# Performance work log

Measured on AMD Instinct MI355X. Metric: run time of the kernel, lower is better.

## Reference

```python
import jax, jax.numpy as jnp
import numpy as np

D_MODEL = 1024
STATE_DIM = 128


def setup_inputs() -> dict:
    key = jax.random.key(0)
    ks = jax.random.split(key, 8)
    B, T, D, N = 8, 4096, D_MODEL, STATE_DIM
    u = jax.random.normal(ks[0], (B, T, D), dtype=jnp.float32)
    h0 = jnp.zeros((B, N), dtype=jnp.float32)
    log_A = jax.random.normal(ks[1], (N,), dtype=jnp.float32) * 0.1 - 1.0
    B_w = jax.random.normal(ks[2], (N, D), dtype=jnp.float32) / np.sqrt(D)
    B_b = jax.random.normal(ks[3], (N,), dtype=jnp.float32) * 0.01
    C_w = jax.random.normal(ks[4], (D, N), dtype=jnp.float32) / np.sqrt(N)
    C_b = jax.random.normal(ks[5], (D,), dtype=jnp.float32) * 0.01
    D_param = jnp.ones((D,), dtype=jnp.float32) * 0.1
    log_dt = jax.random.normal(ks[6], (N,), dtype=jnp.float32) * 0.1 - 2.0
    return {"u": u, "h0": h0, "log_A": log_A, "B_w": B_w, "B_b": B_b,
            "C_w": C_w, "C_b": C_b, "D_param": D_param, "log_dt": log_dt}


def reference(u, h0, log_A, B_w, B_b, C_w, C_b, D_param, log_dt):
    # u: [B, T, D], h0: [B, N]
    dt = jnp.minimum(jnp.exp(log_dt), 1.0)          # [N]
    A = -jnp.exp(log_A)                             # [N]
    A_bar = jnp.exp(A * dt)                         # [N]
    # B_bar * u, precomputed for all timesteps: [B, T, N]
    Bu = (jnp.einsum('btd,nd->btn', u, B_w) + B_b) * dt

    def step(h, bu_t):
        h = A_bar * h + bu_t                        # [B, N]
        return h, h

    # scan over time: Bu transposed to [T, B, N]
    _, hs = jax.lax.scan(step, h0, jnp.swapaxes(Bu, 0, 1))
    hs = jnp.swapaxes(hs, 0, 1)                     # [B, T, N]
    # y = C h + c_bias + D * u
    y = jnp.einsum('btn,dn->btd', hs, C_w) + C_b + D_param * u
    return y
```

## Files before the change

### kernel.cpp

```cpp
#include <hip/hip_runtime.h>

#define B_SZ 8
#define T_SZ 4096
#define D_SZ 1024
#define N_SZ 128
#define M_SZ (B_SZ*T_SZ)
#define CHUNK 64
#define NCHUNK (T_SZ/CHUNK)

typedef __attribute__((ext_vector_type(8))) __bf16 bf16x8;
typedef __attribute__((ext_vector_type(4))) float f32x4;
typedef __attribute__((ext_vector_type(4))) unsigned int u32x4;
typedef __attribute__((ext_vector_type(4))) float fvec4;

static __device__ __forceinline__ unsigned short f2bf(float f){
  union { float f; unsigned int u; } v; v.f = f;
  unsigned int r = v.u + 0x7fffu + ((v.u >> 16) & 1u);
  return (unsigned short)(r >> 16);
}

static __device__ __forceinline__ float bf2f(unsigned short s){
  union { unsigned int u; float f; } v; v.u = ((unsigned)s) << 16;
  return v.f;
}

static __device__ __forceinline__ void cp16(const void* g, void* l){
  __builtin_amdgcn_global_load_lds(
      (const __attribute__((address_space(1))) void*)g,
      (__attribute__((address_space(3))) void*)l, 16, 0, 0);
}

static __device__ __forceinline__ f32x4 zero4(){
  f32x4 v = {0.f, 0.f, 0.f, 0.f};
  return v;
}

__global__ __launch_bounds__(256) void k_conv(const float* __restrict__ Bw,
                                              const float* __restrict__ Cw,
                                              unsigned short* __restrict__ bw,
                                              unsigned short* __restrict__ cw){
  int t = blockIdx.x*256 + threadIdx.x;
  {
    int n = t >> 10, k = t & 1023;
    int c = k >> 6, kk = k & 63;
    unsigned byte = (unsigned)c*16384u + (unsigned)n*128u
                  + (unsigned)((kk*2) ^ ((n&7)<<4));
    bw[byte>>1] = f2bf(Bw[n*1024 + k]);
  }
  {
    int d = t >> 7, k = t & 127;
    int c = d >> 7, dd = d & 127;
    unsigned byte = (unsigned)c*32768u + (unsigned)dd*256u
                  + (unsigned)((k*2) ^ ((dd&15)<<4));
    cw[byte>>1] = f2bf(Cw[d*128 + k]);
  }
}

__global__ __launch_bounds__(256) void k_gemm1c(const float* __restrict__ u,
                                                const unsigned short* __restrict__ bw,
                                                const float* __restrict__ Bb,
                                                const float* __restrict__ logA,
                                                const float* __restrict__ logdt,
                                                unsigned short* __restrict__ Bu_bf,
                                                float* __restrict__ carry){
  __shared__ __align__(16) char smem[32768];
  unsigned short* lA = (unsigned short*)smem;
  unsigned short* lB = (unsigned short*)(smem + 8192);
  float*          BuT = (float*)smem;
  const int tid  = threadIdx.x;
  const int lane = tid & 63;
  const int wave = tid >> 6;
  const int bc   = blockIdx.x;
  const int m0   = bc * 64;
  const int l15  = lane & 15;
  const int lhi  = lane >> 4;

  f32x4 acc[8];
  #pragma unroll
  for (int i=0;i<8;++i) acc[i] = zero4();

  for (int kc=0; kc<16; ++kc){
    #pragma unroll
    for (int rep=0; rep<4; ++rep){
      const char* g = (const char*)bw + kc*16384 + rep*4096 + wave*1024 + lane*16;
      char* l = (char*)lB + rep*4096 + wave*1024;
      cp16(g, l);
    }
    #pragma unroll
    for (int rep=0; rep<2; ++rep){
      int q = rep*256 + tid;
      int row = q >> 3, ks = q & 7;
      const float* src = u + (size_t)(m0+row)*1024 + kc*64 + ks*8;
      fvec4 f0 = *(const fvec4*)src;
      fvec4 f1 = *(const fvec4*)(src+4);
      u32x4 p;
      p.x = (unsigned)f2bf(f0.x) | ((unsigned)f2bf(f0.y)<<16);
      p.y = (unsigned)f2bf(f0.z) | ((unsigned)f2bf(f0.w)<<16);
      p.z = (unsigned)f2bf(f1.x) | ((unsigned)f2bf(f1.y)<<16);
      p.w = (unsigned)f2bf(f1.z) | ((unsigned)f2bf(f1.w)<<16);
      unsigned byte = (unsigned)row*128u + (unsigned)((ks*16) ^ ((row&7)<<4));
      *(u32x4*)((char*)lA + byte) = p;
    }
    __syncthreads();
    #pragma unroll
    for (int k0=0; k0<64; k0+=32){
      int arow = wave*16 + l15;
      int ak = k0 + lhi*8;
      bf16x8 af = *(const bf16x8*)((const char*)lA + arow*128 + ((ak*2) ^ ((arow&7)<<4)));
      #pragma unroll
      for (int ct=0; ct<8; ++ct){
        int bn = ct*16 + l15;
        bf16x8 bfv = *(const bf16x8*)((const char*)lB + bn*128 + ((ak*2) ^ ((bn&7)<<4)));
        acc[ct] = __builtin_amdgcn_mfma_f32_16x16x32_bf16(af, bfv, acc[ct], 0, 0, 0);
      }
    }
    __syncthreads();
  }

  #pragma unroll
  for (int ct=0; ct<8; ++ct){
    int n = ct*16 + l15;
    float dt = fminf(__expf(logdt[n]), 1.f);
    float bb = Bb[n];
    #pragma unroll
    for (int r=0;r<4;++r){
      int ml = wave*16 + lhi*4 + r;
      BuT[ml*128 + n] = (acc[ct][r] + bb) * dt;
    }
  }
  __syncthreads();

  #pragma unroll
  for (int i=0;i<4;++i){
    int q = i*256 + tid;
    const float* s = BuT + q*8;
    fvec4 a = *(const fvec4*)s;
    fvec4 b = *(const fvec4*)(s+4);
    u32x4 p;
    p.x = (unsigned)f2bf(a.x) | ((unsigned)f2bf(a.y)<<16);
    p.y = (unsigned)f2bf(a.z) | ((unsigned)f2bf(a.w)<<16);
    p.z = (unsigned)f2bf(b.x) | ((unsigned)f2bf(b.y)<<16);
    p.w = (unsigned)f2bf(b.z) | ((unsigned)f2bf(b.w)<<16);
    *(u32x4*)((char*)Bu_bf + (size_t)bc*16384 + (size_t)q*16) = p;
  }

  if (tid < 128){
    int n = tid;
    float dt = fminf(__expf(logdt[n]), 1.f);
    float Ab = __expf(-__expf(logA[n]) * dt);
    float h = 0.f;
    #pragma unroll 8
    for (int j=0;j<CHUNK;++j) h = fmaf(Ab, h, BuT[j*128 + n]);
    carry[(size_t)bc*128 + n] = h;
  }
}

__global__ __launch_bounds__(256) void k_gemm2s(const unsigned short* __restrict__ Bu_bf,
                                                const float* __restrict__ carry,
                                                const unsigned short* __restrict__ cw,
                                                const float* __restrict__ u,
                                                const float* __restrict__ h0,
                                                const float* __restrict__ Cb,
                                                const float* __restrict__ Dp,
                                                const float* __restrict__ logA,
                                                const float* __restrict__ logdt,
                                                float* __restrict__ y){
  __shared__ __align__(16) unsigned short BuT[64*128];
  __shared__ __align__(16) unsigned short hsT[64*128];
  __shared__ __align__(16) unsigned short cwT[128*128];
  const int tid = threadIdx.x, lane = tid & 63, wave = tid >> 6;
  const int bc = blockIdx.x;
  const int m0 = bc * 64;
  const int l15 = lane & 15, lhi = lane >> 4;

  #pragma unroll
  for (int i=0;i<4;++i){
    int off = i*4096 + tid*16;
    cp16((const char*)Bu_bf + (size_t)bc*16384 + off, (char*)BuT + off);
  }
  #pragma unroll
  for (int i=0;i<8;++i){
    int off = i*4096 + tid*16;
    cp16((const char*)cw + off, (char*)cwT + off);
  }

  float hreg = 0.f, Ab = 0.f;
  if (tid < 128){
    int n = tid;
    int b = bc >> 6, c = bc & 63;
    float dt = fminf(__expf(logdt[n]), 1.f);
    float Ad = -__expf(logA[n]) * dt;
    Ab = __expf(Ad);
    float AL = __expf(Ad * (float)CHUNK);
    float h = h0[b*128 + n];
    for (int i=0;i<c;++i)
      h = fmaf(AL, h, carry[(size_t)(b*NCHUNK + i)*128 + n]);
    hreg = h;
  }
  __syncthreads();

  if (tid < 128){
    int n = tid;
    float h = hreg;
    #pragma unroll 8
    for (int j=0;j<CHUNK;++j){
      h = fmaf(Ab, h, bf2f(BuT[j*128 + n]));
      unsigned byte = (unsigned)j*256u + (unsigned)((n*2) ^ ((j&15)<<4));
      *(unsigned short*)((char*)hsT + byte) = f2bf(h);
    }
  }
  __syncthreads();

  for (int d=0; d<8; ++d){
    f32x4 acc[8];
    #pragma unroll
    for (int i=0;i<8;++i) acc[i] = zero4();

    #pragma unroll
    for (int k0=0;k0<128;k0+=32){
      int arow = wave*16 + l15;
      int ak = k0 + lhi*8;
      bf16x8 af = *(const bf16x8*)((const char*)hsT + arow*256 + ((ak*2) ^ ((arow&15)<<4)));
      #pragma unroll
      for (int ct=0;ct<8;++ct){
        int dn = ct*16 + l15;
        bf16x8 bfv = *(const bf16x8*)((const char*)cwT + dn*256 + ((ak*2) ^ ((dn&15)<<4)));
        acc[ct] = __builtin_amdgcn_mfma_f32_16x16x32_bf16(af, bfv, acc[ct], 0, 0, 0);
      }
    }
    __syncthreads();

    if (d < 7){
      #pragma unroll
      for (int i=0;i<8;++i){
        int off = (wave*8 + i)*1024 + lane*16;
        cp16((const char*)cw + (size_t)(d+1)*32768 + off, (char*)cwT + off);
      }
    }

    const int d0 = d*128;
    #pragma unroll
    for (int ct=0;ct<8;++ct){
      int dc = d0 + ct*16 + l15;
      float cb = Cb[dc], dp = Dp[dc];
      #pragma unroll
      for (int r=0;r<4;++r){
        int m = m0 + wave*16 + lhi*4 + r;
        size_t off = (size_t)m*1024 + dc;
        y[off] = acc[ct][r] + cb + dp*u[off];
      }
    }
    __syncthreads();
  }
}

extern "C" void kernel_launch(void* const* d_in, const int* in_sizes, int n_in,
                              void* d_out, int out_size, void* d_ws, size_t ws_size,
                              hipStream_t stream){
  (void)in_sizes; (void)n_in; (void)out_size; (void)ws_size;
  const float* u     = (const float*)d_in[0];
  const float* h0    = (const float*)d_in[1];
  const float* logA  = (const float*)d_in[2];
  const float* Bw    = (const float*)d_in[3];
  const float* Bb    = (const float*)d_in[4];
  const float* Cw    = (const float*)d_in[5];
  const float* Cb    = (const float*)d_in[6];
  const float* Dp    = (const float*)d_in[7];
  const float* logdt = (const float*)d_in[8];
  float* y = (float*)d_out;

  char* ws = (char*)d_ws;
  unsigned short* Bu_bf = (unsigned short*)(ws);
  float*          carry = (float*)(ws + 8388608);
  unsigned short* bw    = (unsigned short*)(ws + 8650752);
  unsigned short* cw    = (unsigned short*)(ws + 8912896);

  k_conv  <<<dim3(512), dim3(256), 0, stream>>>(Bw, Cw, bw, cw);
  k_gemm1c<<<dim3(512), dim3(256), 0, stream>>>(u, bw, Bb, logA, logdt, Bu_bf, carry);
  k_gemm2s<<<dim3(512), dim3(256), 0, stream>>>(Bu_bf, carry, cw, u, h0, Cb, Dp,
                                                logA, logdt, y);
}
```

Measured before the change: 87.88 us.

## Drop Bu LDS staging, batch carry loads, prefetch u before MFMA

```diff
diff --git a/kernel.cpp b/kernel.cpp
--- a/kernel.cpp
+++ b/kernel.cpp
@@ -155,7 +155,8 @@
   }
 }
 
-__global__ __launch_bounds__(256) void k_gemm2s(const unsigned short* __restrict__ Bu_bf,
+__global__ __launch_bounds__(256, 3) void k_gemm2s(
+                                                const unsigned short* __restrict__ Bu_bf,
                                                 const float* __restrict__ carry,
                                                 const unsigned short* __restrict__ cw,
                                                 const float* __restrict__ u,
@@ -165,7 +166,6 @@
                                                 const float* __restrict__ logA,
                                                 const float* __restrict__ logdt,
                                                 float* __restrict__ y){
-  __shared__ __align__(16) unsigned short BuT[64*128];
   __shared__ __align__(16) unsigned short hsT[64*128];
   __shared__ __align__(16) unsigned short cwT[128*128];
   const int tid = threadIdx.x, lane = tid & 63, wave = tid >> 6;
@@ -174,37 +174,35 @@
   const int l15 = lane & 15, lhi = lane >> 4;
 
   #pragma unroll
-  for (int i=0;i<4;++i){
-    int off = i*4096 + tid*16;
-    cp16((const char*)Bu_bf + (size_t)bc*16384 + off, (char*)BuT + off);
-  }
-  #pragma unroll
   for (int i=0;i<8;++i){
     int off = i*4096 + tid*16;
     cp16((const char*)cw + off, (char*)cwT + off);
   }
 
-  float hreg = 0.f, Ab = 0.f;
   if (tid < 128){
     int n = tid;
     int b = bc >> 6, c = bc & 63;
     float dt = fminf(__expf(logdt[n]), 1.f);
     float Ad = -__expf(logA[n]) * dt;
-    Ab = __expf(Ad);
+    float Ab = __expf(Ad);
     float AL = __expf(Ad * (float)CHUNK);
     float h = h0[b*128 + n];
-    for (int i=0;i<c;++i)
-      h = fmaf(AL, h, carry[(size_t)(b*NCHUNK + i)*128 + n]);
-    hreg = h;
-  }
-  __syncthreads();
-
-  if (tid < 128){
-    int n = tid;
-    float h = hreg;
+    const float* cp = carry + (size_t)b*NCHUNK*128 + n;
+    #pragma unroll
+    for (int g=0; g<4; ++g){
+      float cbuf[16];
+      #pragma unroll
+      for (int i=0;i<16;++i) cbuf[i] = cp[(size_t)(g*16+i)*128];
+      #pragma unroll
+      for (int i=0;i<16;++i){
+        int idx = g*16 + i;
+        h = (idx < c) ? fmaf(AL, h, cbuf[i]) : h;
+      }
+    }
+    const unsigned short* bp = Bu_bf + (size_t)bc*8192 + n;
     #pragma unroll 8
     for (int j=0;j<CHUNK;++j){
-      h = fmaf(Ab, h, bf2f(BuT[j*128 + n]));
+      h = fmaf(Ab, h, bf2f(bp[(size_t)j*128]));
       unsigned byte = (unsigned)j*256u + (unsigned)((n*2) ^ ((j&15)<<4));
       *(unsigned short*)((char*)hsT + byte) = f2bf(h);
     }
@@ -212,6 +210,19 @@
   __syncthreads();
 
   for (int d=0; d<8; ++d){
+    const int d0 = d*128;
+
+    float upre[8][4];
+    #pragma unroll
+    for (int ct=0;ct<8;++ct){
+      int dc = d0 + ct*16 + l15;
+      #pragma unroll
+      for (int r=0;r<4;++r){
+        int m = m0 + wave*16 + lhi*4 + r;
+        upre[ct][r] = u[(size_t)m*1024 + dc];
+      }
+    }
+
     f32x4 acc[8];
     #pragma unroll
     for (int i=0;i<8;++i) acc[i] = zero4();
@@ -238,7 +249,6 @@
       }
     }
 
-    const int d0 = d*128;
     #pragma unroll
     for (int ct=0;ct<8;++ct){
       int dc = d0 + ct*16 + l15;
@@ -247,7 +257,7 @@
       for (int r=0;r<4;++r){
         int m = m0 + wave*16 + lhi*4 + r;
         size_t off = (size_t)m*1024 + dc;
-        y[off] = acc[ct][r] + cb + dp*u[off];
+        y[off] = acc[ct][r] + cb + dp*upre[ct][r];
       }
     }
     __syncthreads();
```

Measured after the change: 89.17 us. About the same (+1.5%).

## Split GEMM1 and GEMM2 blocks finer to double grid size and occupancy

Applied to the files above, without the earlier changes.

```diff
diff --git a/kernel.cpp b/kernel.cpp
--- a/kernel.cpp
+++ b/kernel.cpp
@@ -5,8 +5,10 @@
 #define D_SZ 1024
 #define N_SZ 128
 #define M_SZ (B_SZ*T_SZ)
-#define CHUNK 64
-#define NCHUNK (T_SZ/CHUNK)
+#define C1 32
+#define NC1 (T_SZ/C1)
+#define C2 64
+#define NC2 (T_SZ/C2)
 
 typedef __attribute__((ext_vector_type(8))) __bf16 bf16x8;
 typedef __attribute__((ext_vector_type(4))) float f32x4;
@@ -32,6 +34,13 @@
 
 static __device__ __forceinline__ f32x4 zero4(){
   f32x4 v = {0.f, 0.f, 0.f, 0.f};
+  return v;
+}
+
+static __device__ __forceinline__ bf16x8 pack8(fvec4 a, fvec4 b){
+  bf16x8 v;
+  v[0]=(__bf16)a.x; v[1]=(__bf16)a.y; v[2]=(__bf16)a.z; v[3]=(__bf16)a.w;
+  v[4]=(__bf16)b.x; v[5]=(__bf16)b.y; v[6]=(__bf16)b.z; v[7]=(__bf16)b.w;
   return v;
 }
 
@@ -56,82 +65,76 @@
   }
 }
 
-__global__ __launch_bounds__(256) void k_gemm1c(const float* __restrict__ u,
-                                                const unsigned short* __restrict__ bw,
-                                                const float* __restrict__ Bb,
-                                                const float* __restrict__ logA,
-                                                const float* __restrict__ logdt,
-                                                unsigned short* __restrict__ Bu_bf,
-                                                float* __restrict__ carry){
-  __shared__ __align__(16) char smem[32768];
+__global__ __launch_bounds__(256, 4) void k_gemm1c(const float* __restrict__ u,
+                                                   const unsigned short* __restrict__ bw,
+                                                   const float* __restrict__ Bb,
+                                                   const float* __restrict__ logA,
+                                                   const float* __restrict__ logdt,
+                                                   unsigned short* __restrict__ Bu_bf,
+                                                   float* __restrict__ carry){
+  __shared__ __align__(16) char smem[20480];
   unsigned short* lA = (unsigned short*)smem;
-  unsigned short* lB = (unsigned short*)(smem + 8192);
+  unsigned short* lB = (unsigned short*)(smem + 4096);
   float*          BuT = (float*)smem;
   const int tid  = threadIdx.x;
   const int lane = tid & 63;
   const int wave = tid >> 6;
   const int bc   = blockIdx.x;
-  const int m0   = bc * 64;
+  const int m0   = bc * 32;
   const int l15  = lane & 15;
   const int lhi  = lane >> 4;
-
-  f32x4 acc[8];
-  #pragma unroll
-  for (int i=0;i<8;++i) acc[i] = zero4();
+  const int rt   = (wave & 1) * 16;
+  const int ct0  = (wave >> 1) * 4;
+
+  f32x4 acc[4];
+  #pragma unroll
+  for (int i=0;i<4;++i) acc[i] = zero4();
 
   for (int kc=0; kc<16; ++kc){
     #pragma unroll
     for (int rep=0; rep<4; ++rep){
-      const char* g = (const char*)bw + kc*16384 + rep*4096 + wave*1024 + lane*16;
-      char* l = (char*)lB + rep*4096 + wave*1024;
-      cp16(g, l);
-    }
-    #pragma unroll
-    for (int rep=0; rep<2; ++rep){
-      int q = rep*256 + tid;
-      int row = q >> 3, ks = q & 7;
+      const char* g = (const char*)bw + kc*16384 + rep*4096 + tid*16;
+      cp16(g, (char*)lB + rep*4096 + tid*16);
+    }
+    {
+      int row = tid >> 3, ks = tid & 7;
       const float* src = u + (size_t)(m0+row)*1024 + kc*64 + ks*8;
       fvec4 f0 = *(const fvec4*)src;
       fvec4 f1 = *(const fvec4*)(src+4);
-      u32x4 p;
-      p.x = (unsigned)f2bf(f0.x) | ((unsigned)f2bf(f0.y)<<16);
-      p.y = (unsigned)f2bf(f0.z) | ((unsigned)f2bf(f0.w)<<16);
-      p.z = (unsigned)f2bf(f1.x) | ((unsigned)f2bf(f1.y)<<16);
-      p.w = (unsigned)f2bf(f1.z) | ((unsigned)f2bf(f1.w)<<16);
       unsigned byte = (unsigned)row*128u + (unsigned)((ks*16) ^ ((row&7)<<4));
-      *(u32x4*)((char*)lA + byte) = p;
+      *(bf16x8*)((char*)lA + byte) = pack8(f0, f1);
     }
     __syncthreads();
     #pragma unroll
     for (int k0=0; k0<64; k0+=32){
-      int arow = wave*16 + l15;
+      int arow = rt + l15;
       int ak = k0 + lhi*8;
       bf16x8 af = *(const bf16x8*)((const char*)lA + arow*128 + ((ak*2) ^ ((arow&7)<<4)));
       #pragma unroll
-      for (int ct=0; ct<8; ++ct){
-        int bn = ct*16 + l15;
+      for (int j=0;j<4;++j){
+        int bn = (ct0+j)*16 + l15;
         bf16x8 bfv = *(const bf16x8*)((const char*)lB + bn*128 + ((ak*2) ^ ((bn&7)<<4)));
-        acc[ct] = __builtin_amdgcn_mfma_f32_16x16x32_bf16(af, bfv, acc[ct], 0, 0, 0);
+        acc[j] = __builtin_amdgcn_mfma_f32_16x16x32_bf16(af, bfv, acc[j], 0, 0, 0);
       }
     }
     __syncthreads();
   }
 
   #pragma unroll
-  for (int ct=0; ct<8; ++ct){
-    int n = ct*16 + l15;
+  for (int j=0;j<4;++j){
+    int n = (ct0+j)*16 + l15;
     float dt = fminf(__expf(logdt[n]), 1.f);
     float bb = Bb[n];
     #pragma unroll
     for (int r=0;r<4;++r){
-      int ml = wave*16 + lhi*4 + r;
-      BuT[ml*128 + n] = (acc[ct][r] + bb) * dt;
+      int ml = rt + lhi*4 + r;
+      BuT[ml*128 + n] = (acc[j][r] + bb) * dt;
     }
   }
   __syncthreads();
 
   #pragma unroll
-  for (int i=0;i<4;++i){
+  for (int i=0;i<2;++i){
     int q = i*256 + tid;
     const float* s = BuT + q*8;
     fvec4 a = *(const fvec4*)s;
@@ -141,7 +144,7 @@
     p.y = (unsigned)f2bf(a.z) | ((unsigned)f2bf(a.w)<<16);
     p.z = (unsigned)f2bf(b.x) | ((unsigned)f2bf(b.y)<<16);
     p.w = (unsigned)f2bf(b.z) | ((unsigned)f2bf(b.w)<<16);
-    *(u32x4*)((char*)Bu_bf + (size_t)bc*16384 + (size_t)q*16) = p;
+    *(u32x4*)((char*)Bu_bf + (size_t)bc*8192 + (size_t)q*16) = p;
   }
 
   if (tid < 128){
@@ -150,12 +153,13 @@
     float Ab = __expf(-__expf(logA[n]) * dt);
     float h = 0.f;
     #pragma unroll 8
-    for (int j=0;j<CHUNK;++j) h = fmaf(Ab, h, BuT[j*128 + n]);
+    for (int j=0;j<C1;++j) h = fmaf(Ab, h, BuT[j*128 + n]);
     carry[(size_t)bc*128 + n] = h;
   }
 }
 
-__global__ __launch_bounds__(256) void k_gemm2s(const unsigned short* __restrict__ Bu_bf,
+__global__ __launch_bounds__(256, 4) void k_gemm2s(
+                                                const unsigned short* __restrict__ Bu_bf,
                                                 const float* __restrict__ carry,
                                                 const unsigned short* __restrict__ cw,
                                                 const float* __restrict__ u,
@@ -167,10 +171,11 @@
                                                 float* __restrict__ y){
   __shared__ __align__(16) unsigned short BuT[64*128];
   __shared__ __align__(16) unsigned short hsT[64*128];
-  __shared__ __align__(16) unsigned short cwT[128*128];
   const int tid = threadIdx.x, lane = tid & 63, wave = tid >> 6;
-  const int bc = blockIdx.x;
-  const int m0 = bc * 64;
+  const int bid = blockIdx.x;
+  const int bc  = bid >> 1;
+  const int dh  = bid & 1;
+  const int m0  = bc * 64;
   const int l15 = lane & 15, lhi = lane >> 4;
 
   #pragma unroll
@@ -178,23 +183,29 @@
     int off = i*4096 + tid*16;
     cp16((const char*)Bu_bf + (size_t)bc*16384 + off, (char*)BuT + off);
   }
-  #pragma unroll
-  for (int i=0;i<8;++i){
-    int off = i*4096 + tid*16;
-    cp16((const char*)cw + off, (char*)cwT + off);
-  }
 
   float hreg = 0.f, Ab = 0.f;
   if (tid < 128){
     int n = tid;
-    int b = bc >> 6, c = bc & 63;
+    int b = bc >> 6;
+    int c32 = (bc & 63) * 2;
     float dt = fminf(__expf(logdt[n]), 1.f);
     float Ad = -__expf(logA[n]) * dt;
     Ab = __expf(Ad);
-    float AL = __expf(Ad * (float)CHUNK);
+    float AL = __expf(Ad * (float)C1);
     float h = h0[b*128 + n];
-    for (int i=0;i<c;++i)
-      h = fmaf(AL, h, carry[(size_t)(b*NCHUNK + i)*128 + n]);
+    const float* cp = carry + (size_t)b*NC1*128 + n;
+    for (int g=0; g<8; ++g){
+      if (g*16 >= c32) break;
+      float cbuf[16];
+      #pragma unroll
+      for (int i=0;i<16;++i) cbuf[i] = cp[(size_t)(g*16+i)*128];
+      #pragma unroll
+      for (int i=0;i<16;++i){
+        int idx = g*16 + i;
+        h = (idx < c32) ? fmaf(AL, h, cbuf[i]) : h;
+      }
+    }
     hreg = h;
   }
   __syncthreads();
@@ -203,7 +214,7 @@
     int n = tid;
     float h = hreg;
     #pragma unroll 8
-    for (int j=0;j<CHUNK;++j){
+    for (int j=0;j<C2;++j){
       h = fmaf(Ab, h, bf2f(BuT[j*128 + n]));
       unsigned byte = (unsigned)j*256u + (unsigned)((n*2) ^ ((j&15)<<4));
       *(unsigned short*)((char*)hsT + byte) = f2bf(h);
@@ -211,46 +222,51 @@
   }
   __syncthreads();
 
-  for (int d=0; d<8; ++d){
-    f32x4 acc[8];
-    #pragma unroll
-    for (int i=0;i<8;++i) acc[i] = zero4();
+  for (int dc4=0; dc4<4; ++dc4){
+    const int d = dh*4 + dc4;
+    const char* cwd = (const char*)cw + (size_t)d*32768;
+
+    f32x4 acc[4][2];
+    #pragma unroll
+    for (int i=0;i<4;++i)
+      #pragma unroll
+      for (int j=0;j<2;++j) acc[i][j] = zero4();
 
     #pragma unroll
     for (int k0=0;k0<128;k0+=32){
-      int arow = wave*16 + l15;
       int ak = k0 + lhi*8;
-      bf16x8 af = *(const bf16x8*)((const char*)hsT + arow*256 + ((ak*2) ^ ((arow&15)<<4)));
-      #pragma unroll
-      for (int ct=0;ct<8;++ct){
-        int dn = ct*16 + l15;
-        bf16x8 bfv = *(const bf16x8*)((const char*)cwT + dn*256 + ((ak*2) ^ ((dn&15)<<4)));
-        acc[ct] = __builtin_amdgcn_mfma_f32_16x16x32_bf16(af, bfv, acc[ct], 0, 0, 0);
-      }
-    }
-    __syncthreads();
-
-    if (d < 7){
-      #pragma unroll
-      for (int i=0;i<8;++i){
-        int off = (wave*8 + i)*1024 + lane*16;
-        cp16((const char*)cw + (size_t)(d+1)*32768 + off, (char*)cwT + off);
+      bf16x8 af[4];
+      #pragma unroll
+      for (int mt=0;mt<4;++mt){
+        int arow = mt*16 + l15;
+        af[mt] = *(const bf16x8*)((const char*)hsT + arow*256 + ((ak*2) ^ ((arow&15)<<4)));
+      }
+      #pragma unroll
+      for (int dt=0;dt<2;++dt){
+        int dn = (wave*2 + dt)*16 + l15;
+        bf16x8 bfv = *(const bf16x8*)(cwd + dn*256 + ((ak*2) ^ ((dn&15)<<4)));
+        #pragma unroll
+        for (int mt=0;mt<4;++mt)
+          acc[mt][dt] = __builtin_amdgcn_mfma_f32_16x16x32_bf16(af[mt], bfv,
+                                                                acc[mt][dt], 0, 0, 0);
       }
     }
 
     const int d0 = d*128;
     #pragma unroll
-    for (int ct=0;ct<8;++ct){
-      int dc = d0 + ct*16 + l15;
-      float cb = Cb[dc], dp = Dp[dc];
-      #pragma unroll
-      for (int r=0;r<4;++r){
-        int m = m0 + wave*16 + lhi*4 + r;
-        size_t off = (size_t)m*1024 + dc;
-        y[off] = acc[ct][r] + cb + dp*u[off];
-      }
-    }
-    __syncthreads();
+    for (int dt=0;dt<2;++dt){
+      int dcol = d0 + (wave*2 + dt)*16 + l15;
+      float cb = Cb[dcol], dp = Dp[dcol];
+      #pragma unroll
+      for (int mt=0;mt<4;++mt){
+        #pragma unroll
+        for (int r=0;r<4;++r){
+          int m = m0 + mt*16 + lhi*4 + r;
+          size_t off = (size_t)m*1024 + dcol;
+          y[off] = acc[mt][dt][r] + cb + dp*u[off];
+        }
+      }
+    }
   }
 }
 
@@ -272,11 +288,11 @@
   char* ws = (char*)d_ws;
   unsigned short* Bu_bf = (unsigned short*)(ws);
   float*          carry = (float*)(ws + 8388608);
-  unsigned short* bw    = (unsigned short*)(ws + 8650752);
-  unsigned short* cw    = (unsigned short*)(ws + 8912896);
-
-  k_conv  <<<dim3(512), dim3(256), 0, stream>>>(Bw, Cw, bw, cw);
-  k_gemm1c<<<dim3(512), dim3(256), 0, stream>>>(u, bw, Bb, logA, logdt, Bu_bf, carry);
-  k_gemm2s<<<dim3(512), dim3(256), 0, stream>>>(Bu_bf, carry, cw, u, h0, Cb, Dp,
-                                                logA, logdt, y);
-}
+  unsigned short* bw    = (unsigned short*)(ws + 8912896);
+  unsigned short* cw    = (unsigned short*)(ws + 9175040);
+
+  k_conv  <<<dim3(512),  dim3(256), 0, stream>>>(Bw, Cw, bw, cw);
+  k_gemm1c<<<dim3(1024), dim3(256), 0, stream>>>(u, bw, Bb, logA, logdt, Bu_bf, carry);
+  k_gemm2s<<<dim3(1024), dim3(256), 0, stream>>>(Bu_bf, carry, cw, u, h0, Cb, Dp,
+                                                 logA, logdt, y);
+}
```

Result: slower. 175.1 us (+99.2%).

## Split output GEMM across two blocks per chunk and cut shared memory footprint

Applied to the files above, without the earlier changes.

```diff
diff --git a/kernel.cpp b/kernel.cpp
--- a/kernel.cpp
+++ b/kernel.cpp
@@ -155,7 +155,8 @@
   }
 }
 
-__global__ __launch_bounds__(256) void k_gemm2s(const unsigned short* __restrict__ Bu_bf,
+__global__ __launch_bounds__(256, 4) void k_gemm2s(
+                                                const unsigned short* __restrict__ Bu_bf,
                                                 const float* __restrict__ carry,
                                                 const unsigned short* __restrict__ cw,
                                                 const float* __restrict__ u,
@@ -165,23 +166,21 @@
                                                 const float* __restrict__ logA,
                                                 const float* __restrict__ logdt,
                                                 float* __restrict__ y){
-  __shared__ __align__(16) unsigned short BuT[64*128];
-  __shared__ __align__(16) unsigned short hsT[64*128];
-  __shared__ __align__(16) unsigned short cwT[128*128];
+  __shared__ __align__(16) char smem[32768];
+  unsigned short* BuT = (unsigned short*)smem;
+  unsigned short* hsT = (unsigned short*)(smem + 16384);
+  unsigned short* cwT = (unsigned short*)smem;
   const int tid = threadIdx.x, lane = tid & 63, wave = tid >> 6;
-  const int bc = blockIdx.x;
-  const int m0 = bc * 64;
+  const int bid = blockIdx.x;
+  const int bc  = bid >> 1;
+  const int dh  = bid & 1;
+  const int m0  = bc * 64;
   const int l15 = lane & 15, lhi = lane >> 4;
 
   #pragma unroll
   for (int i=0;i<4;++i){
     int off = i*4096 + tid*16;
     cp16((const char*)Bu_bf + (size_t)bc*16384 + off, (char*)BuT + off);
-  }
-  #pragma unroll
-  for (int i=0;i<8;++i){
-    int off = i*4096 + tid*16;
-    cp16((const char*)cw + off, (char*)cwT + off);
   }
 
   float hreg = 0.f, Ab = 0.f;
@@ -193,8 +192,18 @@
     Ab = __expf(Ad);
     float AL = __expf(Ad * (float)CHUNK);
     float h = h0[b*128 + n];
-    for (int i=0;i<c;++i)
-      h = fmaf(AL, h, carry[(size_t)(b*NCHUNK + i)*128 + n]);
+    const float* cp = carry + (size_t)b*NCHUNK*128 + n;
+    #pragma unroll
+    for (int g=0; g<4; ++g){
+      float cbuf[16];
+      #pragma unroll
+      for (int i=0;i<16;++i) cbuf[i] = cp[(size_t)(g*16+i)*128];
+      #pragma unroll
+      for (int i=0;i<16;++i){
+        int idx = g*16 + i;
+        h = (idx < c) ? fmaf(AL, h, cbuf[i]) : h;
+      }
+    }
     hreg = h;
   }
   __syncthreads();
@@ -211,26 +220,44 @@
   }
   __syncthreads();
 
-  for (int d=0; d<8; ++d){
+  bf16x8 afr[4];
+  {
+    int arow = wave*16 + l15;
+    #pragma unroll
+    for (int k0i=0;k0i<4;++k0i){
+      int ak = k0i*32 + lhi*8;
+      afr[k0i] = *(const bf16x8*)((const char*)hsT + arow*256 + ((ak*2) ^ ((arow&15)<<4)));
+    }
+  }
+  __syncthreads();
+
+  #pragma unroll
+  for (int i=0;i<8;++i){
+    int off = i*4096 + tid*16;
+    cp16((const char*)cw + (size_t)(dh*4)*32768 + off, (char*)cwT + off);
+  }
+
+  for (int dc4=0; dc4<4; ++dc4){
+    const int d = dh*4 + dc4;
+    __syncthreads();
+
     f32x4 acc[8];
     #pragma unroll
     for (int i=0;i<8;++i) acc[i] = zero4();
 
     #pragma unroll
-    for (int k0=0;k0<128;k0+=32){
-      int arow = wave*16 + l15;
-      int ak = k0 + lhi*8;
-      bf16x8 af = *(const bf16x8*)((const char*)hsT + arow*256 + ((ak*2) ^ ((arow&15)<<4)));
+    for (int k0i=0;k0i<4;++k0i){
+      int ak = k0i*32 + lhi*8;
       #pragma unroll
       for (int ct=0;ct<8;++ct){
-        int dn = ct*16 + l15;
-        bf16x8 bfv = *(const bf16x8*)((const char*)cwT + dn*256 + ((ak*2) ^ ((dn&15)<<4)));
-        acc[ct] = __builtin_amdgcn_mfma_f32_16x16x32_bf16(af, bfv, acc[ct], 0, 0, 0);
+        int bn = ct*16 + l15;
+        bf16x8 bfv = *(const bf16x8*)((const char*)cwT + bn*256 + ((ak*2) ^ ((bn&15)<<4)));
+        acc[ct] = __builtin_amdgcn_mfma_f32_16x16x32_bf16(afr[k0i], bfv, acc[ct], 0, 0, 0);
       }
     }
     __syncthreads();
 
-    if (d < 7){
+    if (dc4 < 3){
       #pragma unroll
       for (int i=0;i<8;++i){
         int off = (wave*8 + i)*1024 + lane*16;
@@ -250,7 +277,6 @@
         y[off] = acc[ct][r] + cb + dp*u[off];
       }
     }
-    __syncthreads();
   }
 }
 
@@ -275,8 +301,8 @@
   unsigned short* bw    = (unsigned short*)(ws + 8650752);
   unsigned short* cw    = (unsigned short*)(ws + 8912896);
 
-  k_conv  <<<dim3(512), dim3(256), 0, stream>>>(Bw, Cw, bw, cw);
-  k_gemm1c<<<dim3(512), dim3(256), 0, stream>>>(u, bw, Bb, logA, logdt, Bu_bf, carry);
-  k_gemm2s<<<dim3(512), dim3(256), 0, stream>>>(Bu_bf, carry, cw, u, h0, Cb, Dp,
-                                                logA, logdt, y);
-}
+  k_conv  <<<dim3(512),  dim3(256), 0, stream>>>(Bw, Cw, bw, cw);
+  k_gemm1c<<<dim3(512),  dim3(256), 0, stream>>>(u, bw, Bb, logA, logdt, Bu_bf, carry);
+  k_gemm2s<<<dim3(1024), dim3(256), 0, stream>>>(Bu_bf, carry, cw, u, h0, Cb, Dp,
+                                                 logA, logdt, y);
+}
```

Measured after the change: 90.38 us. 1.03x slower.
